# Optimization experiments

Hardware: AMD Instinct MI355X
Metric: run time of the kernel (lower is better)

## Reference

```python
import jax, jax.numpy as jnp
import numpy as np

NUM_EMBEDDINGS = 512
EMBEDDING_DIM = 64
COMMITMENT_COST = 0.25


def setup_inputs() -> dict:
    key = jax.random.key(0)
    k1, k2 = jax.random.split(key)
    z_e = jax.random.normal(k1, (16, EMBEDDING_DIM, 64, 64), dtype=jnp.float32)
    # embedding.weight initialized uniform(-1/K, 1/K) in the torch module
    lim = 1.0 / NUM_EMBEDDINGS
    embedding = jax.random.uniform(
        k2, (NUM_EMBEDDINGS, EMBEDDING_DIM), dtype=jnp.float32,
        minval=-lim, maxval=lim)
    return {"z_e": z_e, "embedding": embedding}


def reference(z_e, embedding):
    b, c, h, w = z_e.shape
    K = embedding.shape[0]
    # NCHW -> NHWC -> [N, D]
    flat = jnp.transpose(z_e, (0, 2, 3, 1)).reshape(-1, c)  # [N, D]
    distances = (jnp.sum(flat * flat, axis=1, keepdims=True)
                 + jnp.sum(embedding * embedding, axis=1)
                 - 2.0 * jnp.matmul(flat, embedding.T))
    encoding_indices = jnp.argmin(distances, axis=1)  # [N]
    # one_hot @ embedding == gather (same math, avoids materializing [N,K] fp mm)
    z_q_flat = jnp.take(embedding, encoding_indices, axis=0)  # [N, D]
    z_q = jnp.transpose(z_q_flat.reshape(b, h, w, c), (0, 3, 1, 2))  # NCHW
    # EMA codebook: only commitment loss, codes updated via EMA (detached)
    e_latent_loss = jnp.mean((jax.lax.stop_gradient(z_q) - z_e) ** 2)
    loss = COMMITMENT_COST * e_latent_loss
    # straight-through estimator
    z_q_st = z_e + jax.lax.stop_gradient(z_q - z_e)
    # perplexity from one-hot assignment frequencies
    counts = jnp.zeros((K,), dtype=jnp.float32).at[encoding_indices].add(1.0)
    avg_probs = counts / flat.shape[0]
    perplexity = jnp.exp(-jnp.sum(avg_probs * jnp.log(avg_probs + 1e-10)))
    return z_q_st, loss, perplexity, encoding_indices
```

## Files before the change

kernel.cpp:

```cpp
#include <hip/hip_runtime.h>

#define BATCH 16
#define CH 64
#define HW 4096
#define NPIX 65536
#define KCODES 512
#define DDIM 64
#define NELEM 4194304

#define OUT_LOSS 4194304
#define OUT_PPL  4194305
#define OUT_IDX  4194306

#define MARGIN 2.2e-4f

typedef short bf16x8 __attribute__((ext_vector_type(8)));
typedef float f32x4  __attribute__((ext_vector_type(4)));

__device__ __forceinline__ float rnd(float s) {
    asm volatile("" : "+v"(s));
    return s;
}
__device__ __forceinline__ short f2bf(float f) {
    unsigned u = __builtin_bit_cast(unsigned, f);
    unsigned r = (u + 0x7fffu + ((u >> 16) & 1u)) >> 16;
    return (short)r;
}
__device__ __forceinline__ void gl_lds16(const void* g, void* l) {
    __builtin_amdgcn_global_load_lds(
        (const __attribute__((address_space(1))) unsigned*)g,
        (__attribute__((address_space(3))) unsigned*)l, 16, 0, 0);
}

__global__ void k_prep(const float* __restrict__ emb, float* __restrict__ e2,
                       bf16x8* __restrict__ Bh, float4* __restrict__ P4) {
    int gid = blockIdx.x * 256 + threadIdx.x;
    if (gid < 4096) {
        int tn = gid >> 7, rem = gid & 127;
        int chunk = (rem >> 6) & 1, q = (rem >> 4) & 3, i = rem & 15;
        int code = tn * 16 + i;
        const float* src = emb + code * DDIM + chunk * 32 + q * 8;
        bf16x8 h;
        #pragma unroll
        for (int j = 0; j < 8; ++j) h[j] = f2bf(src[j]);
        Bh[gid] = h;
    } else if (gid < 4608) {
        int k = gid - 4096;
        const float* row = emb + k * DDIM;
        float r[8];
        #pragma unroll
        for (int j = 0; j < 8; ++j) { float v = row[j]; r[j] = rnd(v * v); }
        #pragma unroll
        for (int m = 1; m < 8; ++m)
            #pragma unroll
            for (int j = 0; j < 8; ++j) { float v = row[8 * m + j]; r[j] += rnd(v * v); }
        e2[k] = ((r[0] + r[1]) + (r[2] + r[3])) + ((r[4] + r[5]) + (r[6] + r[7]));
    } else if (gid < 12800) {
        int pid = gid - 4608;
        int kk = pid >> 10, c4 = (pid >> 6) & 15, lane = pid & 63;
        int code = lane * 8 + kk;
        P4[pid] = *(const float4*)(emb + code * DDIM + c4 * 4);
    }
}

__global__ __launch_bounds__(512, 4) void k_dist(
        const float* __restrict__ z_e, const float* __restrict__ emb,
        const bf16x8* __restrict__ Bh, const float* __restrict__ e2g,
        int* __restrict__ idx, int* __restrict__ glist, int* __restrict__ nflag,
        int* __restrict__ counts, float* __restrict__ slots,
        float* __restrict__ out) {
    __shared__ bf16x8 Bs[4096];
    __shared__ float e2s[512];
    __shared__ int   hist[512];
    __shared__ int   flist[128];
    __shared__ int   fcnt, fbase;

    int t = threadIdx.x;
    int pxbase = blockIdx.x * 128;
    int batch = pxbase >> 12;
    int p0 = pxbase & 4095;
    const float* zb = z_e + (size_t)batch * (CH * HW) + p0;

    #pragma unroll
    for (int i = 0; i < 8; ++i) gl_lds16(Bh + i * 512 + t, Bs + i * 512 + t);

    hist[t] = 0;
    e2s[t] = e2g[t];
    if (t == 0) fcnt = 0;

    int w = t >> 6, lane = t & 63, col = lane & 15, quad = lane >> 4;
    int px = w * 16 + col;

    bf16x8 a0, a1;
    #pragma unroll
    for (int j = 0; j < 8; ++j) {
        a0[j] = f2bf(zb[(quad * 8 + j) * HW + px]);
        a1[j] = f2bf(zb[(32 + quad * 8 + j) * HW + px]);
    }
    __syncthreads();

    float m1[4], m2[4];
    int   i1[4];
    #pragma unroll
    for (int r = 0; r < 4; ++r) { m1[r] = 1e30f; m2[r] = 1e30f; i1[r] = 0; }

    #pragma unroll 4
    for (int tn = 0; tn < 32; ++tn) {
        bf16x8 c0 = Bs[tn * 128 + lane];
        bf16x8 c1 = Bs[tn * 128 + 64 + lane];
        float e2v = e2s[tn * 16 + col];
        int n = tn * 16 + col;
        f32x4 acc = {0.f, 0.f, 0.f, 0.f};
        acc = __builtin_amdgcn_mfma_f32_16x16x32_bf16(a0, c0, acc, 0, 0, 0);
        acc = __builtin_amdgcn_mfma_f32_16x16x32_bf16(a1, c1, acc, 0, 0, 0);
        #pragma unroll
        for (int r = 0; r < 4; ++r) {
            float d = fmaf(-2.0f, acc[r], e2v);
            m2[r] = __builtin_amdgcn_fmed3f(d, m1[r], m2[r]);
            bool c = d < m1[r];
            m1[r] = fminf(d, m1[r]);
            i1[r] = c ? n : i1[r];
        }
    }

    #pragma unroll
    for (int off = 1; off < 16; off <<= 1) {
        #pragma unroll
        for (int r = 0; r < 4; ++r) {
            float om1 = __shfl_xor(m1[r], off);
            float om2 = __shfl_xor(m2[r], off);
            int   oi  = __shfl_xor(i1[r], off);
            if (om1 < m1[r] || (om1 == m1[r] && oi < i1[r])) {
                m2[r] = fminf(m1[r], om2);
                m1[r] = om1;
                i1[r] = oi;
            } else {
                m2[r] = fminf(m2[r], om1);
            }
        }
    }

    if (col == 0) {
        #pragma unroll
        for (int r = 0; r < 4; ++r) {
            int g = pxbase + w * 16 + quad * 4 + r;
            idx[g] = i1[r];
            out[OUT_IDX + g] = (float)i1[r];
            atomicAdd(&hist[i1[r]], 1);
            if (m2[r] - m1[r] < MARGIN) {
                int pos = atomicAdd(&fcnt, 1);
                flist[pos] = g;
            }
        }
    }

    int q4 = lane & 3;
    int bidx[4];
    #pragma unroll
    for (int j = 0; j < 4; ++j) bidx[j] = __shfl(i1[j], q4 << 4);
    const float* zw = zb + w * 16;
    float* ow = out + (size_t)batch * (CH * HW) + p0 + w * 16;
    float lsum = 0.0f;
    #pragma unroll
    for (int it = 0; it < 4; ++it) {
        int c = it * 16 + (lane >> 2);
        float4 ze = *(const float4*)(zw + c * HW + q4 * 4);
        float d0 = emb[bidx[0] * DDIM + c] - ze.x;
        float d1 = emb[bidx[1] * DDIM + c] - ze.y;
        float d2 = emb[bidx[2] * DDIM + c] - ze.z;
        float d3 = emb[bidx[3] * DDIM + c] - ze.w;
        float4 o = {ze.x + d0, ze.y + d1, ze.z + d2, ze.w + d3};
        *(float4*)(ow + c * HW + q4 * 4) = o;
        lsum = lsum + d0 * d0 + d1 * d1 + d2 * d2 + d3 * d3;
    }
    #pragma unroll
    for (int off = 32; off; off >>= 1) lsum += __shfl_down(lsum, off);
    if (lane == 0) atomicAdd(&slots[((blockIdx.x * 8 + w) & 63) * 16], lsum);

    __syncthreads();
    int v0 = hist[t];
    if (v0) atomicAdd(&counts[t], v0);
    if (t == 0) fbase = atomicAdd(nflag, fcnt);
    __syncthreads();
    if (t < fcnt) glist[fbase + t] = flist[t];
}

__global__ __launch_bounds__(256) void k_refine(
        const float* __restrict__ z_e, const float* __restrict__ emb,
        const float* __restrict__ e2, const float4* __restrict__ P4,
        const int* __restrict__ glist, const int* __restrict__ nflag,
        int* __restrict__ idx, int* __restrict__ counts,
        float* __restrict__ slots, float* __restrict__ out) {
    __shared__ float4 Ps[8192];
    __shared__ float  xs[4][64];

    int t = threadIdx.x;
    int w = t >> 6, lane = t & 63;
    int n = nflag[0];
    if (blockIdx.x >= n) return;

    #pragma unroll
    for (int i = 0; i < 32; ++i) gl_lds16(P4 + i * 256 + t, Ps + i * 256 + t);
    __syncthreads();

    float4 ea = ((const float4*)e2)[lane * 2];
    float4 eb = ((const float4*)e2)[lane * 2 + 1];
    float e2v[8] = {ea.x, ea.y, ea.z, ea.w, eb.x, eb.y, eb.z, eb.w};

    int wid = blockIdx.x * 4 + w;
    for (int j = wid; j < n; j += 1024) {
        int g = glist[j];
        int b = g >> 12, p = g & 4095;
        xs[w][lane] = z_e[(size_t)b * (CH * HW) + (size_t)lane * HW + p];
        __threadfence_block();

        const float* xr = xs[w];
        float r[8];
        #pragma unroll
        for (int jj = 0; jj < 8; ++jj) { float v = xr[jj]; r[jj] = rnd(v * v); }
        #pragma unroll
        for (int mm = 1; mm < 8; ++mm)
            #pragma unroll
            for (int jj = 0; jj < 8; ++jj) { float v = xr[8 * mm + jj]; r[jj] += rnd(v * v); }
        float x2 = ((r[0] + r[1]) + (r[2] + r[3])) + ((r[4] + r[5]) + (r[6] + r[7]));

        float bestd = INFINITY;
        int besti = 1 << 30;
        #pragma unroll
        for (int kk = 0; kk < 8; ++kk) {
            double d0 = 0.0, d1 = 0.0, d2 = 0.0, d3 = 0.0;
            #pragma unroll
            for (int c4 = 0; c4 < 16; ++c4) {
                float4 xq = *(const float4*)&xr[c4 * 4];
                float4 ev = Ps[(kk * 16 + c4) * 64 + lane];
                d0 = fma((double)xq.x, (double)ev.x, d0);
                d1 = fma((double)xq.y, (double)ev.y, d1);
                d2 = fma((double)xq.z, (double)ev.z, d2);
                d3 = fma((double)xq.w, (double)ev.w, d3);
            }
            float dotf = (float)((d0 + d1) + (d2 + d3));
            float tt = x2 + e2v[kk];
            float d = tt - 2.0f * dotf;
            if (d < bestd) { bestd = d; besti = lane * 8 + kk; }
        }
        #pragma unroll
        for (int off = 32; off; off >>= 1) {
            float od = __shfl_down(bestd, off);
            int   oi = __shfl_down(besti, off);
            if (od < bestd || (od == bestd && oi < besti)) { bestd = od; besti = oi; }
        }
        besti = __shfl(besti, 0);

        int old = idx[g];
        if (besti != old) {
            float xc = xr[lane];
            float qn = emb[besti * DDIM + lane];
            float qo = emb[old * DDIM + lane];
            float dn = qn - xc, dold = qo - xc;
            out[(size_t)b * (CH * HW) + (size_t)lane * HW + p] = xc + dn;
            float delta = dn * dn - dold * dold;
            #pragma unroll
            for (int off = 32; off; off >>= 1) delta += __shfl_down(delta, off);
            if (lane == 0) {
                atomicAdd(&slots[(wid & 63) * 16], delta);
                atomicAdd(&counts[old], -1);
                atomicAdd(&counts[besti], 1);
                idx[g] = besti;
                out[OUT_IDX + g] = (float)besti;
            }
        }
    }
}

__global__ void k_final(const int* __restrict__ counts,
                        const float* __restrict__ slots,
                        float* __restrict__ out) {
    int t = threadIdx.x;
    float cnt = (float)counts[t];
    float pb = cnt * (1.0f / 65536.0f);
    float term = pb * logf(pb + 1e-10f);
    #pragma unroll
    for (int off = 32; off; off >>= 1) term += __shfl_down(term, off);
    __shared__ float ls[8];
    __shared__ float lsum;
    int lane = t & 63, w = t >> 6;
    if (lane == 0) ls[w] = term;
    if (w == 0) {
        float s2 = slots[lane * 16];
        #pragma unroll
        for (int off = 32; off; off >>= 1) s2 += __shfl_down(s2, off);
        if (lane == 0) lsum = s2;
    }
    __syncthreads();
    if (t == 0) {
        float s = 0.0f;
        #pragma unroll
        for (int i = 0; i < 8; ++i) s += ls[i];
        out[OUT_PPL]  = expf(-s);
        out[OUT_LOSS] = 0.25f * (lsum / (float)NELEM);
    }
}

extern "C" void kernel_launch(void* const* d_in, const int* in_sizes, int n_in,
                              void* d_out, int out_size, void* d_ws, size_t ws_size,
                              hipStream_t stream) {
    const float* z_e = (const float*)d_in[0];
    const float* emb = (const float*)d_in[1];
    float* out = (float*)d_out;
    char* ws = (char*)d_ws;

    int*    idx    = (int*)(ws);
    int*    glist  = (int*)(ws + 262144);
    float*  e2     = (float*)(ws + 524288);
    int*    nflag  = (int*)(ws + 526336);
    int*    counts = (int*)(ws + 526400);
    float*  slots  = (float*)(ws + 528448);
    bf16x8* Bh     = (bf16x8*)(ws + 532544);
    float4* P4     = (float4*)(ws + 598080);

    hipMemsetAsync(ws + 526336, 0, 532544 - 526336, stream);

    k_prep<<<50, 256, 0, stream>>>(emb, e2, Bh, P4);
    k_dist<<<NPIX / 128, 512, 0, stream>>>(z_e, emb, Bh, e2, idx, glist, nflag, counts, slots, out);
    k_refine<<<256, 256, 0, stream>>>(z_e, emb, e2, P4, glist, nflag, idx, counts, slots, out);
    k_final<<<1, 512, 0, stream>>>(counts, slots, out);
}
```

Baseline: 128.9 us.

## Fuse codebook prep into dist/refine kernels and fold final reduction into refine

```diff
diff --git a/kernel.cpp b/kernel.cpp
--- a/kernel.cpp
+++ b/kernel.cpp
@@ -26,46 +26,9 @@
     unsigned r = (u + 0x7fffu + ((u >> 16) & 1u)) >> 16;
     return (short)r;
 }
-__device__ __forceinline__ void gl_lds16(const void* g, void* l) {
-    __builtin_amdgcn_global_load_lds(
-        (const __attribute__((address_space(1))) unsigned*)g,
-        (__attribute__((address_space(3))) unsigned*)l, 16, 0, 0);
-}
-
-__global__ void k_prep(const float* __restrict__ emb, float* __restrict__ e2,
-                       bf16x8* __restrict__ Bh, float4* __restrict__ P4) {
-    int gid = blockIdx.x * 256 + threadIdx.x;
-    if (gid < 4096) {
-        int tn = gid >> 7, rem = gid & 127;
-        int chunk = (rem >> 6) & 1, q = (rem >> 4) & 3, i = rem & 15;
-        int code = tn * 16 + i;
-        const float* src = emb + code * DDIM + chunk * 32 + q * 8;
-        bf16x8 h;
-        #pragma unroll
-        for (int j = 0; j < 8; ++j) h[j] = f2bf(src[j]);
-        Bh[gid] = h;
-    } else if (gid < 4608) {
-        int k = gid - 4096;
-        const float* row = emb + k * DDIM;
-        float r[8];
-        #pragma unroll
-        for (int j = 0; j < 8; ++j) { float v = row[j]; r[j] = rnd(v * v); }
-        #pragma unroll
-        for (int m = 1; m < 8; ++m)
-            #pragma unroll
-            for (int j = 0; j < 8; ++j) { float v = row[8 * m + j]; r[j] += rnd(v * v); }
-        e2[k] = ((r[0] + r[1]) + (r[2] + r[3])) + ((r[4] + r[5]) + (r[6] + r[7]));
-    } else if (gid < 12800) {
-        int pid = gid - 4608;
-        int kk = pid >> 10, c4 = (pid >> 6) & 15, lane = pid & 63;
-        int code = lane * 8 + kk;
-        P4[pid] = *(const float4*)(emb + code * DDIM + c4 * 4);
-    }
-}
 
 __global__ __launch_bounds__(512, 4) void k_dist(
         const float* __restrict__ z_e, const float* __restrict__ emb,
-        const bf16x8* __restrict__ Bh, const float* __restrict__ e2g,
         int* __restrict__ idx, int* __restrict__ glist, int* __restrict__ nflag,
         int* __restrict__ counts, float* __restrict__ slots,
         float* __restrict__ out) {
@@ -82,10 +45,30 @@
     const float* zb = z_e + (size_t)batch * (CH * HW) + p0;
 
     #pragma unroll
-    for (int i = 0; i < 8; ++i) gl_lds16(Bh + i * 512 + t, Bs + i * 512 + t);
-
+    for (int i8 = 0; i8 < 8; ++i8) {
+        int gid = i8 * 512 + t;
+        int tn = gid >> 7, rem = gid & 127;
+        int chunk = (rem >> 6) & 1, q = (rem >> 4) & 3, ii = rem & 15;
+        const float* src = emb + (tn * 16 + ii) * DDIM + chunk * 32 + q * 8;
+        float4 v0 = *(const float4*)src;
+        float4 v1 = *(const float4*)(src + 4);
+        bf16x8 h;
+        h[0] = f2bf(v0.x); h[1] = f2bf(v0.y); h[2] = f2bf(v0.z); h[3] = f2bf(v0.w);
+        h[4] = f2bf(v1.x); h[5] = f2bf(v1.y); h[6] = f2bf(v1.z); h[7] = f2bf(v1.w);
+        Bs[gid] = h;
+    }
+    {
+        const float* row = emb + t * DDIM;
+        float r[8];
+        #pragma unroll
+        for (int j = 0; j < 8; ++j) { float v = row[j]; r[j] = rnd(v * v); }
+        #pragma unroll
+        for (int m = 1; m < 8; ++m)
+            #pragma unroll
+            for (int j = 0; j < 8; ++j) { float v = row[8 * m + j]; r[j] += rnd(v * v); }
+        e2s[t] = ((r[0] + r[1]) + (r[2] + r[3])) + ((r[4] + r[5]) + (r[6] + r[7]));
+    }
     hist[t] = 0;
-    e2s[t] = e2g[t];
     if (t == 0) fcnt = 0;
 
     int w = t >> 6, lane = t & 63, col = lane & 15, quad = lane >> 4;
@@ -187,25 +170,48 @@
 
 __global__ __launch_bounds__(256) void k_refine(
         const float* __restrict__ z_e, const float* __restrict__ emb,
-        const float* __restrict__ e2, const float4* __restrict__ P4,
         const int* __restrict__ glist, const int* __restrict__ nflag,
         int* __restrict__ idx, int* __restrict__ counts,
-        float* __restrict__ slots, float* __restrict__ out) {
+        float* __restrict__ slots, int* __restrict__ done,
+        float* __restrict__ out) {
     __shared__ float4 Ps[8192];
     __shared__ float  xs[4][64];
+    __shared__ int    islast;
+    __shared__ float  ls[4];
+    __shared__ float  lsumf;
 
     int t = threadIdx.x;
     int w = t >> 6, lane = t & 63;
     int n = nflag[0];
-    if (blockIdx.x >= n) return;
-
-    #pragma unroll
-    for (int i = 0; i < 32; ++i) gl_lds16(P4 + i * 256 + t, Ps + i * 256 + t);
-    __syncthreads();
-
-    float4 ea = ((const float4*)e2)[lane * 2];
-    float4 eb = ((const float4*)e2)[lane * 2 + 1];
-    float e2v[8] = {ea.x, ea.y, ea.z, ea.w, eb.x, eb.y, eb.z, eb.w};
+
+    #pragma unroll
+    for (int it = 0; it < 32; ++it) {
+        int e = it * 256 + t;
+        int ln = e & 63, c4 = (e >> 6) & 15, kk = e >> 10;
+        Ps[e] = *(const float4*)(emb + (ln * 8 + kk) * DDIM + c4 * 4);
+    }
+    __syncthreads();
+
+    float e2v[8];
+    #pragma unroll
+    for (int kk = 0; kk < 8; ++kk) {
+        float4 ev = Ps[(kk * 16 + 0) * 64 + lane];
+        float rA0 = rnd(ev.x * ev.x), rA1 = rnd(ev.y * ev.y);
+        float rA2 = rnd(ev.z * ev.z), rA3 = rnd(ev.w * ev.w);
+        ev = Ps[(kk * 16 + 1) * 64 + lane];
+        float rB0 = rnd(ev.x * ev.x), rB1 = rnd(ev.y * ev.y);
+        float rB2 = rnd(ev.z * ev.z), rB3 = rnd(ev.w * ev.w);
+        #pragma unroll
+        for (int m = 1; m < 8; ++m) {
+            ev = Ps[(kk * 16 + 2 * m) * 64 + lane];
+            rA0 += rnd(ev.x * ev.x); rA1 += rnd(ev.y * ev.y);
+            rA2 += rnd(ev.z * ev.z); rA3 += rnd(ev.w * ev.w);
+            ev = Ps[(kk * 16 + 2 * m + 1) * 64 + lane];
+            rB0 += rnd(ev.x * ev.x); rB1 += rnd(ev.y * ev.y);
+            rB2 += rnd(ev.z * ev.z); rB3 += rnd(ev.w * ev.w);
+        }
+        e2v[kk] = ((rA0 + rA1) + (rA2 + rA3)) + ((rB0 + rB1) + (rB2 + rB3));
+    }
 
     int wid = blockIdx.x * 4 + w;
     for (int j = wid; j < n; j += 1024) {
@@ -270,34 +276,38 @@
             }
         }
     }
-}
-
-__global__ void k_final(const int* __restrict__ counts,
-                        const float* __restrict__ slots,
-                        float* __restrict__ out) {
-    int t = threadIdx.x;
-    float cnt = (float)counts[t];
-    float pb = cnt * (1.0f / 65536.0f);
-    float term = pb * logf(pb + 1e-10f);
+
+    __syncthreads();
+    if (t == 0) {
+        __threadfence();
+        int d = atomicAdd(done, 1);
+        islast = (d == (int)gridDim.x - 1);
+    }
+    __syncthreads();
+    if (!islast) return;
+
+    float term = 0.0f;
+    #pragma unroll
+    for (int h = 0; h < 2; ++h) {
+        int c = h * 256 + t;
+        float cnt = (float)atomicAdd(&counts[c], 0);
+        float pb = cnt * (1.0f / 65536.0f);
+        term += pb * logf(pb + 1e-10f);
+    }
     #pragma unroll
     for (int off = 32; off; off >>= 1) term += __shfl_down(term, off);
-    __shared__ float ls[8];
-    __shared__ float lsum;
-    int lane = t & 63, w = t >> 6;
     if (lane == 0) ls[w] = term;
     if (w == 0) {
-        float s2 = slots[lane * 16];
+        float s2 = atomicAdd(&slots[lane * 16], 0.0f);
         #pragma unroll
         for (int off = 32; off; off >>= 1) s2 += __shfl_down(s2, off);
-        if (lane == 0) lsum = s2;
+        if (lane == 0) lsumf = s2;
     }
     __syncthreads();
     if (t == 0) {
-        float s = 0.0f;
-        #pragma unroll
-        for (int i = 0; i < 8; ++i) s += ls[i];
+        float s = ls[0] + ls[1] + ls[2] + ls[3];
         out[OUT_PPL]  = expf(-s);
-        out[OUT_LOSS] = 0.25f * (lsum / (float)NELEM);
+        out[OUT_LOSS] = 0.25f * (lsumf / (float)NELEM);
     }
 }
 
@@ -309,19 +319,15 @@
     float* out = (float*)d_out;
     char* ws = (char*)d_ws;
 
-    int*    idx    = (int*)(ws);
-    int*    glist  = (int*)(ws + 262144);
-    float*  e2     = (float*)(ws + 524288);
-    int*    nflag  = (int*)(ws + 526336);
-    int*    counts = (int*)(ws + 526400);
-    float*  slots  = (float*)(ws + 528448);
-    bf16x8* Bh     = (bf16x8*)(ws + 532544);
-    float4* P4     = (float4*)(ws + 598080);
-
-    hipMemsetAsync(ws + 526336, 0, 532544 - 526336, stream);
-
-    k_prep<<<50, 256, 0, stream>>>(emb, e2, Bh, P4);
-    k_dist<<<NPIX / 128, 512, 0, stream>>>(z_e, emb, Bh, e2, idx, glist, nflag, counts, slots, out);
-    k_refine<<<256, 256, 0, stream>>>(z_e, emb, e2, P4, glist, nflag, idx, counts, slots, out);
-    k_final<<<1, 512, 0, stream>>>(counts, slots, out);
-}
+    int*   idx    = (int*)(ws);
+    int*   glist  = (int*)(ws + 262144);
+    int*   nflag  = (int*)(ws + 524288);
+    int*   counts = (int*)(ws + 524352);
+    float* slots  = (float*)(ws + 526400);
+    int*   done   = (int*)(ws + 530496);
+
+    hipMemsetAsync(ws + 524288, 0, 530560 - 524288, stream);
+
+    k_dist<<<NPIX / 128, 512, 0, stream>>>(z_e, emb, idx, glist, nflag, counts, slots, out);
+    k_refine<<<256, 256, 0, stream>>>(z_e, emb, glist, nflag, idx, counts, slots, done, out);
+}
```

Measured after the change: 205.7 us. +59.6%, slower.

## Fold workspace memset into prep kernel and final reduction into refine via last-block

Applied to the files above, without the earlier changes.

```diff
diff --git a/kernel.cpp b/kernel.cpp
--- a/kernel.cpp
+++ b/kernel.cpp
@@ -33,7 +33,12 @@
 }
 
 __global__ void k_prep(const float* __restrict__ emb, float* __restrict__ e2,
-                       bf16x8* __restrict__ Bh, float4* __restrict__ P4) {
+                       bf16x8* __restrict__ Bh, float4* __restrict__ P4,
+                       int* __restrict__ zws) {
+    if (blockIdx.x == 0) {
+        #pragma unroll
+        for (int i = threadIdx.x; i < 1568; i += 256) zws[i] = 0;
+    }
     int gid = blockIdx.x * 256 + threadIdx.x;
     if (gid < 4096) {
         int tn = gid >> 7, rem = gid & 127;
@@ -190,114 +195,123 @@
         const float* __restrict__ e2, const float4* __restrict__ P4,
         const int* __restrict__ glist, const int* __restrict__ nflag,
         int* __restrict__ idx, int* __restrict__ counts,
-        float* __restrict__ slots, float* __restrict__ out) {
+        float* __restrict__ slots, int* __restrict__ done,
+        float* __restrict__ out) {
     __shared__ float4 Ps[8192];
     __shared__ float  xs[4][64];
+    __shared__ int    islast;
+    __shared__ float  ls[4];
+    __shared__ float  lsumf;
 
     int t = threadIdx.x;
     int w = t >> 6, lane = t & 63;
     int n = nflag[0];
-    if (blockIdx.x >= n) return;
-
-    #pragma unroll
-    for (int i = 0; i < 32; ++i) gl_lds16(P4 + i * 256 + t, Ps + i * 256 + t);
-    __syncthreads();
-
-    float4 ea = ((const float4*)e2)[lane * 2];
-    float4 eb = ((const float4*)e2)[lane * 2 + 1];
-    float e2v[8] = {ea.x, ea.y, ea.z, ea.w, eb.x, eb.y, eb.z, eb.w};
-
-    int wid = blockIdx.x * 4 + w;
-    for (int j = wid; j < n; j += 1024) {
-        int g = glist[j];
-        int b = g >> 12, p = g & 4095;
-        xs[w][lane] = z_e[(size_t)b * (CH * HW) + (size_t)lane * HW + p];
-        __threadfence_block();
-
-        const float* xr = xs[w];
-        float r[8];
-        #pragma unroll
-        for (int jj = 0; jj < 8; ++jj) { float v = xr[jj]; r[jj] = rnd(v * v); }
-        #pragma unroll
-        for (int mm = 1; mm < 8; ++mm)
-            #pragma unroll
-            for (int jj = 0; jj < 8; ++jj) { float v = xr[8 * mm + jj]; r[jj] += rnd(v * v); }
-        float x2 = ((r[0] + r[1]) + (r[2] + r[3])) + ((r[4] + r[5]) + (r[6] + r[7]));
-
-        float bestd = INFINITY;
-        int besti = 1 << 30;
-        #pragma unroll
-        for (int kk = 0; kk < 8; ++kk) {
-            double d0 = 0.0, d1 = 0.0, d2 = 0.0, d3 = 0.0;
-            #pragma unroll
-            for (int c4 = 0; c4 < 16; ++c4) {
-                float4 xq = *(const float4*)&xr[c4 * 4];
-                float4 ev = Ps[(kk * 16 + c4) * 64 + lane];
-                d0 = fma((double)xq.x, (double)ev.x, d0);
-                d1 = fma((double)xq.y, (double)ev.y, d1);
-                d2 = fma((double)xq.z, (double)ev.z, d2);
-                d3 = fma((double)xq.w, (double)ev.w, d3);
-            }
-            float dotf = (float)((d0 + d1) + (d2 + d3));
-            float tt = x2 + e2v[kk];
-            float d = tt - 2.0f * dotf;
-            if (d < bestd) { bestd = d; besti = lane * 8 + kk; }
+
+    if (blockIdx.x * 4 < n) {
+        #pragma unroll
+        for (int i = 0; i < 32; ++i) gl_lds16(P4 + i * 256 + t, Ps + i * 256 + t);
+        __syncthreads();
+
+        float4 ea = ((const float4*)e2)[lane * 2];
+        float4 eb = ((const float4*)e2)[lane * 2 + 1];
+        float e2v[8] = {ea.x, ea.y, ea.z, ea.w, eb.x, eb.y, eb.z, eb.w};
+
+        int wid = blockIdx.x * 4 + w;
+        for (int j = wid; j < n; j += 1024) {
+            int g = glist[j];
+            int b = g >> 12, p = g & 4095;
+            xs[w][lane] = z_e[(size_t)b * (CH * HW) + (size_t)lane * HW + p];
+            __threadfence_block();
+
+            const float* xr = xs[w];
+            float r[8];
+            #pragma unroll
+            for (int jj = 0; jj < 8; ++jj) { float v = xr[jj]; r[jj] = rnd(v * v); }
+            #pragma unroll
+            for (int mm = 1; mm < 8; ++mm)
+                #pragma unroll
+                for (int jj = 0; jj < 8; ++jj) { float v = xr[8 * mm + jj]; r[jj] += rnd(v * v); }
+            float x2 = ((r[0] + r[1]) + (r[2] + r[3])) + ((r[4] + r[5]) + (r[6] + r[7]));
+
+            float bestd = INFINITY;
+            int besti = 1 << 30;
+            #pragma unroll
+            for (int kk = 0; kk < 8; ++kk) {
+                double d0 = 0.0, d1 = 0.0, d2 = 0.0, d3 = 0.0;
+                #pragma unroll
+                for (int c4 = 0; c4 < 16; ++c4) {
+                    float4 xq = *(const float4*)&xr[c4 * 4];
+                    float4 ev = Ps[(kk * 16 + c4) * 64 + lane];
+                    d0 = fma((double)xq.x, (double)ev.x, d0);
+                    d1 = fma((double)xq.y, (double)ev.y, d1);
+                    d2 = fma((double)xq.z, (double)ev.z, d2);
+                    d3 = fma((double)xq.w, (double)ev.w, d3);
+                }
+                float dotf = (float)((d0 + d1) + (d2 + d3));
+                float tt = x2 + e2v[kk];
+                float d = tt - 2.0f * dotf;
+                if (d < bestd) { bestd = d; besti = lane * 8 + kk; }
+            }
+            #pragma unroll
+            for (int off = 32; off; off >>= 1) {
+                float od = __shfl_down(bestd, off);
+                int   oi = __shfl_down(besti, off);
+                if (od < bestd || (od == bestd && oi < besti)) { bestd = od; besti = oi; }
+            }
+            besti = __shfl(besti, 0);
+
+            int old = idx[g];
+            if (besti != old) {
+                float xc = xr[lane];
+                float qn = emb[besti * DDIM + lane];
+                float qo = emb[old * DDIM + lane];
+                float dn = qn - xc, dold = qo - xc;
+                out[(size_t)b * (CH * HW) + (size_t)lane * HW + p] = xc + dn;
+                float delta = dn * dn - dold * dold;
+                #pragma unroll
+                for (int off = 32; off; off >>= 1) delta += __shfl_down(delta, off);
+                if (lane == 0) {
+                    atomicAdd(&slots[(wid & 63) * 16], delta);
+                    atomicAdd(&counts[old], -1);
+                    atomicAdd(&counts[besti], 1);
+                    idx[g] = besti;
+                    out[OUT_IDX + g] = (float)besti;
+                }
+            }
         }
-        #pragma unroll
-        for (int off = 32; off; off >>= 1) {
-            float od = __shfl_down(bestd, off);
-            int   oi = __shfl_down(besti, off);
-            if (od < bestd || (od == bestd && oi < besti)) { bestd = od; besti = oi; }
-        }
-        besti = __shfl(besti, 0);
-
-        int old = idx[g];
-        if (besti != old) {
-            float xc = xr[lane];
-            float qn = emb[besti * DDIM + lane];
-            float qo = emb[old * DDIM + lane];
-            float dn = qn - xc, dold = qo - xc;
-            out[(size_t)b * (CH * HW) + (size_t)lane * HW + p] = xc + dn;
-            float delta = dn * dn - dold * dold;
-            #pragma unroll
-            for (int off = 32; off; off >>= 1) delta += __shfl_down(delta, off);
-            if (lane == 0) {
-                atomicAdd(&slots[(wid & 63) * 16], delta);
-                atomicAdd(&counts[old], -1);
-                atomicAdd(&counts[besti], 1);
-                idx[g] = besti;
-                out[OUT_IDX + g] = (float)besti;
-            }
-        }
-    }
-}
-
-__global__ void k_final(const int* __restrict__ counts,
-                        const float* __restrict__ slots,
-                        float* __restrict__ out) {
-    int t = threadIdx.x;
-    float cnt = (float)counts[t];
-    float pb = cnt * (1.0f / 65536.0f);
-    float term = pb * logf(pb + 1e-10f);
+        __syncthreads();
+    }
+
+    if (t == 0) {
+        __threadfence();
+        int d = atomicAdd(done, 1);
+        islast = (d == (int)gridDim.x - 1);
+    }
+    __syncthreads();
+    if (!islast) return;
+
+    float term = 0.0f;
+    #pragma unroll
+    for (int h = 0; h < 2; ++h) {
+        int c = h * 256 + t;
+        float cnt = (float)atomicAdd(&counts[c], 0);
+        float pb = cnt * (1.0f / 65536.0f);
+        term += pb * logf(pb + 1e-10f);
+    }
     #pragma unroll
     for (int off = 32; off; off >>= 1) term += __shfl_down(term, off);
-    __shared__ float ls[8];
-    __shared__ float lsum;
-    int lane = t & 63, w = t >> 6;
     if (lane == 0) ls[w] = term;
     if (w == 0) {
-        float s2 = slots[lane * 16];
+        float s2 = atomicAdd(&slots[lane * 16], 0.0f);
         #pragma unroll
         for (int off = 32; off; off >>= 1) s2 += __shfl_down(s2, off);
-        if (lane == 0) lsum = s2;
+        if (lane == 0) lsumf = s2;
     }
     __syncthreads();
     if (t == 0) {
-        float s = 0.0f;
-        #pragma unroll
-        for (int i = 0; i < 8; ++i) s += ls[i];
+        float s = ls[0] + ls[1] + ls[2] + ls[3];
         out[OUT_PPL]  = expf(-s);
-        out[OUT_LOSS] = 0.25f * (lsum / (float)NELEM);
+        out[OUT_LOSS] = 0.25f * (lsumf / (float)NELEM);
     }
 }
 
@@ -315,13 +329,13 @@
     int*    nflag  = (int*)(ws + 526336);
     int*    counts = (int*)(ws + 526400);
     float*  slots  = (float*)(ws + 528448);
-    bf16x8* Bh     = (bf16x8*)(ws + 532544);
-    float4* P4     = (float4*)(ws + 598080);
-
-    hipMemsetAsync(ws + 526336, 0, 532544 - 526336, stream);
-
-    k_prep<<<50, 256, 0, stream>>>(emb, e2, Bh, P4);
+    int*    done   = (int*)(ws + 532544);
+    bf16x8* Bh     = (bf16x8*)(ws + 532608);
+    float4* P4     = (float4*)(ws + 598144);
+
+    int* zws = (int*)(ws + 526336);
+
+    k_prep<<<50, 256, 0, stream>>>(emb, e2, Bh, P4, zws);
     k_dist<<<NPIX / 128, 512, 0, stream>>>(z_e, emb, Bh, e2, idx, glist, nflag, counts, slots, out);
-    k_refine<<<256, 256, 0, stream>>>(z_e, emb, e2, P4, glist, nflag, idx, counts, slots, out);
-    k_final<<<1, 512, 0, stream>>>(counts, slots, out);
-}
+    k_refine<<<256, 256, 0, stream>>>(z_e, emb, e2, P4, glist, nflag, idx, counts, slots, done, out);
+}
```

Measured after the change: 130.8 us. Within noise of the previous version (+1.5%).
